# Kernel tuning notes

Hardware: AMD Instinct MI355X
Metric: run time of the kernel (lower is better)

Reference implementation:

```python
import jax, jax.numpy as jnp
import numpy as np

D_MODEL = 1024
NUM_HEADS = 16
D_K = D_MODEL // NUM_HEADS
S, B = 2048, 2


def setup_inputs() -> dict:
    key = jax.random.key(0)
    ks = jax.random.split(key, 11)
    lim = 1.0 / np.sqrt(D_MODEL)
    def lin(kw, kb):
        W = jax.random.uniform(kw, (D_MODEL, D_MODEL), jnp.float32, -lim, lim)
        b = jax.random.uniform(kb, (D_MODEL,), jnp.float32, -lim, lim)
        return W, b
    Wq, bq = lin(ks[0], ks[1])
    Wk, bk = lin(ks[2], ks[3])
    Wv, bv = lin(ks[4], ks[5])
    Wo, bo = lin(ks[6], ks[7])
    q = jax.random.normal(ks[8], (S, B, D_MODEL), jnp.float32)
    k = jax.random.normal(ks[9], (S, B, D_MODEL), jnp.float32)
    v = jax.random.normal(ks[10], (S, B, D_MODEL), jnp.float32)
    return {"q": q, "k": k, "v": v,
            "Wq": Wq, "bq": bq, "Wk": Wk, "bk": bk,
            "Wv": Wv, "bv": bv, "Wo": Wo, "bo": bo}


def reference(q, k, v, Wq, bq, Wk, bk, Wv, bv, Wo, bo):
    s, b, _ = q.shape
    scale = np.sqrt(D_K).astype(np.float32)
    # torch Linear: x @ W.T + b
    def proj(x, W, bias):
        y = jnp.einsum('sbd,ed->sbe', x, W) + bias
        # [S,B,D] -> [B,H,S,d_k]
        return y.reshape(s, b, NUM_HEADS, D_K).transpose(1, 2, 0, 3)
    Q = proj(q, Wq, bq)
    K = proj(k, Wk, bk)
    V = proj(v, Wv, bv)
    scores = jnp.einsum('bhsd,bhtd->bhst', Q, K) / scale  # [B,H,S,S]
    attn = jax.nn.softmax(scores, axis=-1)
    ctx = jnp.einsum('bhst,bhtd->bhsd', attn, V)  # [B,H,S,d_k]
    ctx = ctx.transpose(2, 0, 1, 3).reshape(s, b, NUM_HEADS * D_K)
    return jnp.einsum('sbd,ed->sbe', ctx, Wo) + bo
```

## Files before the change

### kernel.cpp

```cpp
#include <hip/hip_runtime.h>
#include <stdint.h>

typedef __attribute__((ext_vector_type(8))) short short8;
typedef __attribute__((ext_vector_type(4))) float f32x4;
typedef __attribute__((ext_vector_type(16))) float f32x16;

#define MFMA16(a, b, c) __builtin_amdgcn_mfma_f32_16x16x32_bf16((a), (b), (c), 0, 0, 0)
#define MFMA32(a, b, c) __builtin_amdgcn_mfma_f32_32x32x16_bf16((a), (b), (c), 0, 0, 0)

__device__ inline unsigned short f2bf(float x) {
  unsigned u = __float_as_uint(x);
  u = (u + 0x7FFFu + ((u >> 16) & 1u)) >> 16;
  return (unsigned short)u;
}

__device__ inline void gload16(const unsigned short* g, unsigned short* l) {
  __builtin_amdgcn_global_load_lds(
      (const __attribute__((address_space(1))) unsigned int*)g,
      (__attribute__((address_space(3))) unsigned int*)l, 16, 0, 0);
}

__device__ inline short8 lds8(const unsigned short* base, int byteoff) {
  return *reinterpret_cast<const short8*>(reinterpret_cast<const char*>(base) + byteoff);
}

__device__ inline unsigned cvtpk(float lo, float hi) {
  unsigned r;
  asm("v_cvt_pk_bf16_f32 %0, %1, %2" : "=v"(r) : "v"(lo), "v"(hi));
  return r;
}
__device__ inline void plswap(unsigned& a, unsigned& b) {
  asm volatile("v_permlane32_swap_b32 %0, %1" : "+v"(a), "+v"(b));
}

__device__ inline short8 mk8(unsigned a, unsigned b, unsigned c, unsigned d) {
  union { unsigned u[4]; short8 v; } x;
  x.u[0] = a; x.u[1] = b; x.u[2] = c; x.u[3] = d;
  return x.v;
}

__device__ inline int swz(int row, int chunk) {
  return row * 128 + (((chunk) ^ (row & 7)) << 4);
}

__global__ __launch_bounds__(256) void cvt_bf16x(const float* __restrict__ a0,
                                                 const float* __restrict__ a1,
                                                 const float* __restrict__ a2,
                                                 const float* __restrict__ a3,
                                                 unsigned short* __restrict__ d, int per) {
  int y = blockIdx.y;
  const float* s = (y == 0) ? a0 : (y == 1) ? a1 : (y == 2) ? a2 : a3;
  int i = (blockIdx.x * 256 + threadIdx.x) * 8;
  if (i >= per) return;
  float4 v0 = *reinterpret_cast<const float4*>(s + i);
  float4 v1 = *reinterpret_cast<const float4*>(s + i + 4);
  short8 o;
  o[0] = (short)f2bf(v0.x); o[1] = (short)f2bf(v0.y);
  o[2] = (short)f2bf(v0.z); o[3] = (short)f2bf(v0.w);
  o[4] = (short)f2bf(v1.x); o[5] = (short)f2bf(v1.y);
  o[6] = (short)f2bf(v1.z); o[7] = (short)f2bf(v1.w);
  *reinterpret_cast<short8*>(d + (size_t)y * per + i) = o;
}

template <int MODE>
__global__ __launch_bounds__(256) void gemm_bt(
    const unsigned short* __restrict__ Abase, const unsigned short* __restrict__ Wbase,
    const float* __restrict__ bias0, const float* __restrict__ bias1,
    const float* __restrict__ bias2, unsigned short* __restrict__ ObaseBf,
    float* __restrict__ ObaseF, int M, int N, int K) {
  constexpr int CHUNK = (MODE == 0) ? 96 : 32;
  const int orig = blockIdx.x;
  const int wg = (orig & 7) * CHUNK + (orig >> 3);
  int z, bx, by;
  if (MODE == 0) {
    z = wg >> 8; by = (wg >> 5) & 7; bx = wg & 31;
  } else {
    z = 0; by = wg >> 5; bx = wg & 31;
  }

  const unsigned short* A = Abase + (size_t)z * M * K;
  const unsigned short* W = Wbase + (size_t)z * N * K;
  const float* bias = (z == 0) ? bias0 : (z == 1 ? bias1 : bias2);

  __shared__ unsigned short As[128 * 64];
  __shared__ unsigned short Bs[128 * 64];

  const int t = threadIdx.x;
  const int lane = t & 63, w = t >> 6;
  const int wm = w >> 1, wn = w & 1;
  const int m0 = bx * 128, n0 = by * 128;
  const int lrow = lane & 15, lg = lane >> 4;

  f32x4 acc[4][4] = {};

  for (int kt = 0; kt < K; kt += 64) {
    __syncthreads();
#pragma unroll
    for (int p = 0; p < 4; ++p) {
      int ci = (p * 4 + w) * 64;
      int c = ci + lane;
      int row = c >> 3, cc = (c & 7) ^ (row & 7);
      gload16(&A[(size_t)(m0 + row) * K + kt + cc * 8], &As[ci * 8]);
      gload16(&W[(size_t)(n0 + row) * K + kt + cc * 8], &Bs[ci * 8]);
    }
    __syncthreads();
#pragma unroll
    for (int kc = 0; kc < 2; ++kc) {
      short8 af[4], bfr[4];
#pragma unroll
      for (int i = 0; i < 4; ++i) {
        af[i] = *reinterpret_cast<const short8*>((const char*)As + swz(wm * 64 + i * 16 + lrow, kc * 4 + lg));
        bfr[i] = *reinterpret_cast<const short8*>((const char*)Bs + swz(wn * 64 + i * 16 + lrow, kc * 4 + lg));
      }
#pragma unroll
      for (int mi = 0; mi < 4; ++mi)
#pragma unroll
        for (int ni = 0; ni < 4; ++ni) acc[mi][ni] = MFMA16(af[mi], bfr[ni], acc[mi][ni]);
    }
  }

  const int r0 = lg * 4;
  if (MODE == 0) {
    const float scale = (z == 0) ? 0.18033688011112042f : 1.0f;
    if (z < 2) {
      unsigned short* O = ObaseBf + (size_t)z * (size_t)M * N;
#pragma unroll
      for (int mi = 0; mi < 4; ++mi)
#pragma unroll
        for (int ni = 0; ni < 4; ++ni) {
          int e = n0 + wn * 64 + ni * 16 + lrow;
          float be = bias[e];
          int h = e >> 6, d = e & 63;
#pragma unroll
          for (int r = 0; r < 4; ++r) {
            int m = m0 + wm * 64 + mi * 16 + r0 + r;
            int s = m >> 1, bb = m & 1;
            O[(((size_t)(bb * 16 + h) * 2048 + s) << 6) + d] = f2bf((acc[mi][ni][r] + be) * scale);
          }
        }
    } else {
      unsigned short* O = ObaseBf + (size_t)2 * (size_t)M * N;
#pragma unroll
      for (int mi = 0; mi < 4; ++mi)
#pragma unroll
        for (int ni = 0; ni < 4; ++ni) {
          int e = n0 + wn * 64 + ni * 16 + lrow;
          float be = bias[e];
          int h = e >> 6, d = e & 63;
#pragma unroll
          for (int r = 0; r < 4; ++r) {
            int m = m0 + wm * 64 + mi * 16 + r0 + r;
            int s = m >> 1, bb = m & 1;
            O[(((size_t)(bb * 16 + h) * 64 + d) << 11) + s] = f2bf(acc[mi][ni][r] + be);
          }
        }
    }
  } else {
    float* O = ObaseF;
#pragma unroll
    for (int mi = 0; mi < 4; ++mi)
#pragma unroll
      for (int ni = 0; ni < 4; ++ni) {
        int e = n0 + wn * 64 + ni * 16 + lrow;
        float be = bias[e];
#pragma unroll
        for (int r = 0; r < 4; ++r) {
          int m = m0 + wm * 64 + mi * 16 + r0 + r;
          O[(size_t)m * N + e] = acc[mi][ni][r] + be;
        }
      }
  }
}

__global__ __launch_bounds__(256) void attn(const unsigned short* __restrict__ Q,
                                            const unsigned short* __restrict__ K,
                                            const unsigned short* __restrict__ Vt,
                                            unsigned short* __restrict__ ctx) {
  __shared__ unsigned short Ks[4 * 4096];
  __shared__ unsigned short Vs[4 * 4096];

  const int orig = blockIdx.x;
  const int wg = ((orig & 7) << 6) + (orig >> 3);
  const int bh = wg >> 4;
  const int qb = wg & 15;

  const int t = threadIdx.x, lane = t & 63, wv = t >> 6;
  const int q0 = qb * 128 + wv * 32;
  const int q = lane & 31, hi = lane >> 5;
  const int fq = (q ^ (q >> 3)) & 7;

  const unsigned short* Qb = Q + ((size_t)bh * 2048 + q0) * 64;
  const unsigned short* Kb = K + (size_t)bh * 2048 * 64;
  const unsigned short* Vb = Vt + (size_t)bh * 64 * 2048;

  short8 qf[4];
#pragma unroll
  for (int m = 0; m < 4; ++m)
    qf[m] = *reinterpret_cast<const short8*>(&Qb[q * 64 + m * 16 + hi * 8]);

  const short8 ones = {0x3F80, 0x3F80, 0x3F80, 0x3F80, 0x3F80, 0x3F80, 0x3F80, 0x3F80};

  int koff[2][4], voff[2][2][2];
#pragma unroll
  for (int st = 0; st < 2; ++st) {
    int f = fq ^ (st ? 4 : 0);
#pragma unroll
    for (int m = 0; m < 4; ++m)
      koff[st][m] = (st * 32 + q) * 128 + (((m * 2 + hi) ^ f) << 4);
  }
#pragma unroll
  for (int dh = 0; dh < 2; ++dh) {
    int f = fq ^ (dh ? 4 : 0);
#pragma unroll
    for (int st = 0; st < 2; ++st)
#pragma unroll
      for (int kc = 0; kc < 2; ++kc)
        voff[dh][st][kc] = (dh * 32 + q) * 128 + (((st * 4 + kc * 2 + hi) ^ f) << 4);
  }

  int c0 = wv * 64 + lane, c1 = (4 + wv) * 64 + lane;
  int sr0 = c0 >> 3, sr1 = c1 >> 3;
  int sc0c = ((c0 & 7) ^ ((sr0 ^ (sr0 >> 3)) & 7)) * 8;
  int sc1c = ((c1 & 7) ^ ((sr1 ^ (sr1 >> 3)) & 7)) * 8;
  const unsigned short* ks0 = Kb + (size_t)sr0 * 64 + sc0c;
  const unsigned short* ks1 = Kb + (size_t)sr1 * 64 + sc1c;
  const unsigned short* vp0 = Vb + (size_t)sr0 * 2048 + sc0c;
  const unsigned short* vp1 = Vb + (size_t)sr1 * 2048 + sc1c;

  f32x16 oa0 = {}, oa1 = {}, osum = {};

#pragma unroll
  for (int pt = 0; pt < 3; ++pt) {
    char* kb = (char*)Ks + pt * 8192;
    char* vb2 = (char*)Vs + pt * 8192;
    gload16(ks0, (unsigned short*)(kb + wv * 1024));
    gload16(ks1, (unsigned short*)(kb + (4 + wv) * 1024));
    gload16(vp0, (unsigned short*)(vb2 + wv * 1024));
    gload16(vp1, (unsigned short*)(vb2 + (4 + wv) * 1024));
    ks0 += 4096; ks1 += 4096; vp0 += 64; vp1 += 64;
  }

  for (int tile = 0; tile < 32; ++tile) {
    asm volatile("s_waitcnt vmcnt(8)" ::: "memory");
    __builtin_amdgcn_s_barrier();
    __builtin_amdgcn_sched_barrier(0);

    {
      char* kb = (char*)Ks + ((tile + 3) & 3) * 8192;
      char* vb2 = (char*)Vs + ((tile + 3) & 3) * 8192;
      gload16(ks0, (unsigned short*)(kb + wv * 1024));
      gload16(ks1, (unsigned short*)(kb + (4 + wv) * 1024));
      gload16(vp0, (unsigned short*)(vb2 + wv * 1024));
      gload16(vp1, (unsigned short*)(vb2 + (4 + wv) * 1024));
      ks0 += 4096; ks1 += 4096; vp0 += 64; vp1 += 64;
    }

    const int cur = (tile & 3) * 8192;
    __builtin_amdgcn_s_setprio(1);

    f32x16 s0 = {}, s1 = {};
#pragma unroll
    for (int m = 0; m < 4; ++m) {
      short8 k0 = lds8(Ks, cur + koff[0][m]);
      short8 k1 = lds8(Ks, cur + koff[1][m]);
      s0 = MFMA32(k0, qf[m], s0);
      s1 = MFMA32(k1, qf[m], s1);
    }

#pragma unroll
    for (int st = 0; st < 2; ++st) {
      const f32x16& sv = st ? s1 : s0;
      float p[16];
#pragma unroll
      for (int i = 0; i < 16; ++i) p[i] = __builtin_amdgcn_exp2f(sv[i]);

      unsigned w0 = cvtpk(p[0], p[1]), w1 = cvtpk(p[2], p[3]);
      unsigned w2 = cvtpk(p[4], p[5]), w3 = cvtpk(p[6], p[7]);
      plswap(w0, w2); plswap(w1, w3);
      unsigned w4 = cvtpk(p[8], p[9]), w5 = cvtpk(p[10], p[11]);
      unsigned w6 = cvtpk(p[12], p[13]), w7 = cvtpk(p[14], p[15]);
      plswap(w4, w6); plswap(w5, w7);
      short8 pa0 = mk8(w0, w1, w2, w3);
      short8 pa1 = mk8(w4, w5, w6, w7);

      osum = MFMA32(pa0, ones, osum);
      oa0 = MFMA32(pa0, lds8(Vs, cur + voff[0][st][0]), oa0);
      oa1 = MFMA32(pa0, lds8(Vs, cur + voff[1][st][0]), oa1);
      osum = MFMA32(pa1, ones, osum);
      oa0 = MFMA32(pa1, lds8(Vs, cur + voff[0][st][1]), oa0);
      oa1 = MFMA32(pa1, lds8(Vs, cur + voff[1][st][1]), oa1);
    }
    __builtin_amdgcn_s_setprio(0);
  }

  const int b = bh >> 4, h = bh & 15;
#pragma unroll
  for (int r = 0; r < 16; ++r) {
    int qr = (r & 3) + 8 * (r >> 2) + 4 * hi;
    float li = 1.0f / osum[r];
    size_t base = ((size_t)(q0 + qr) * 2 + b) * 1024 + h * 64 + q;
    ctx[base] = f2bf(oa0[r] * li);
    ctx[base + 32] = f2bf(oa1[r] * li);
  }
}

extern "C" void kernel_launch(void* const* d_in, const int* in_sizes, int n_in, void* d_out,
                              int out_size, void* d_ws, size_t ws_size, hipStream_t stream) {
  const float* q  = (const float*)d_in[0];
  const float* k  = (const float*)d_in[1];
  const float* v  = (const float*)d_in[2];
  const float* Wq = (const float*)d_in[3];
  const float* bq = (const float*)d_in[4];
  const float* Wk = (const float*)d_in[5];
  const float* bk = (const float*)d_in[6];
  const float* Wv = (const float*)d_in[7];
  const float* bv = (const float*)d_in[8];
  const float* Wo = (const float*)d_in[9];
  const float* bo = (const float*)d_in[10];

  const size_t SZ_IN = 4194304;
  const size_t SZ_W  = 1048576;
  unsigned short* ws  = (unsigned short*)d_ws;
  unsigned short* xb  = ws;
  unsigned short* Wb  = xb + 3 * SZ_IN;
  unsigned short* QKV = Wb + 4 * SZ_W;
  unsigned short* ctx = QKV + 3 * SZ_IN;

  cvt_bf16x<<<dim3(SZ_IN / 2048, 3), 256, 0, stream>>>(q, k, v, v, xb, (int)SZ_IN);
  cvt_bf16x<<<dim3(SZ_W / 2048, 4), 256, 0, stream>>>(Wq, Wk, Wv, Wo, Wb, (int)SZ_W);

  gemm_bt<0><<<768, 256, 0, stream>>>(xb, Wb, bq, bk, bv, QKV, nullptr, 4096, 1024, 1024);
  attn<<<512, 256, 0, stream>>>(QKV, QKV + SZ_IN, QKV + 2 * SZ_IN, ctx);
  gemm_bt<1><<<256, 256, 0, stream>>>(ctx, Wb + 3 * SZ_W, bo, bo, bo, nullptr,
                                      (float*)d_out, 4096, 1024, 1024);
}
```

Measured before the change: 141.7 us.

## Double-buffer GEMM LDS tiles and halve output GEMM tile width

The GEMM kernel now double-buffers its LDS tiles, issuing the next K-slice's global-to-LDS loads before the MFMA work on the current slice, with one barrier per iteration instead of two. The output projection uses 128x64 tiles and a grid of 512 blocks instead of 256, which puts more workgroups across the CUs. The cost is twice the LDS per block, which may lower occupancy, plus one wasted prefetch of slice 0 on the final iteration. The MODE 1 block mapping is also changed (by = wg>>5 now covers 16 column tiles), and it stays consistent with the new CHUNK of 64.

```diff
diff --git a/kernel.cpp b/kernel.cpp
--- a/kernel.cpp
+++ b/kernel.cpp
@@ -68,7 +68,11 @@
     const float* __restrict__ bias0, const float* __restrict__ bias1,
     const float* __restrict__ bias2, unsigned short* __restrict__ ObaseBf,
     float* __restrict__ ObaseF, int M, int N, int K) {
-  constexpr int CHUNK = (MODE == 0) ? 96 : 32;
+  constexpr int BN = (MODE == 0) ? 128 : 64;
+  constexpr int WN = BN / 32;
+  constexpr int CB = BN / 32;
+  constexpr int CHUNK = (MODE == 0) ? 96 : 64;
+
   const int orig = blockIdx.x;
   const int wg = (orig & 7) * CHUNK + (orig >> 3);
   int z, bx, by;
@@ -82,42 +86,70 @@
   const unsigned short* W = Wbase + (size_t)z * N * K;
   const float* bias = (z == 0) ? bias0 : (z == 1 ? bias1 : bias2);
 
-  __shared__ unsigned short As[128 * 64];
-  __shared__ unsigned short Bs[128 * 64];
+  __shared__ unsigned short As[2 * 128 * 64];
+  __shared__ unsigned short Bs[2 * BN * 64];
 
   const int t = threadIdx.x;
   const int lane = t & 63, w = t >> 6;
   const int wm = w >> 1, wn = w & 1;
-  const int m0 = bx * 128, n0 = by * 128;
+  const int m0 = bx * 128, n0 = by * BN;
   const int lrow = lane & 15, lg = lane >> 4;
 
-  f32x4 acc[4][4] = {};
-
+  f32x4 acc[4][WN] = {};
+
+  int arow[4], acol[4], brow[CB], bcol[CB];
+#pragma unroll
+  for (int p = 0; p < 4; ++p) {
+    int c = (p * 4 + w) * 64 + lane;
+    arow[p] = c >> 3; acol[p] = ((c & 7) ^ (arow[p] & 7)) * 8;
+  }
+#pragma unroll
+  for (int p = 0; p < CB; ++p) {
+    int c = (p * 4 + w) * 64 + lane;
+    brow[p] = c >> 3; bcol[p] = ((c & 7) ^ (brow[p] & 7)) * 8;
+  }
+
+#define STAGE_G(kt, buf)                                                              \
+  {                                                                                   \
+    _Pragma("unroll") for (int p = 0; p < 4; ++p)                                     \
+        gload16(&A[(size_t)(m0 + arow[p]) * K + (kt) + acol[p]],                      \
+                &As[(buf)*8192 + ((p * 4 + w) * 64) * 8]);                            \
+    _Pragma("unroll") for (int p = 0; p < CB; ++p)                                    \
+        gload16(&W[(size_t)(n0 + brow[p]) * K + (kt) + bcol[p]],                      \
+                &Bs[(buf)*BN * 64 + ((p * 4 + w) * 64) * 8]);                         \
+  }
+
+  STAGE_G(0, 0);
+  asm volatile("s_waitcnt vmcnt(0)" ::: "memory");
+  __builtin_amdgcn_s_barrier();
+  __builtin_amdgcn_sched_barrier(0);
+
+  int cur = 0;
   for (int kt = 0; kt < K; kt += 64) {
-    __syncthreads();
-#pragma unroll
-    for (int p = 0; p < 4; ++p) {
-      int ci = (p * 4 + w) * 64;
-      int c = ci + lane;
-      int row = c >> 3, cc = (c & 7) ^ (row & 7);
-      gload16(&A[(size_t)(m0 + row) * K + kt + cc * 8], &As[ci * 8]);
-      gload16(&W[(size_t)(n0 + row) * K + kt + cc * 8], &Bs[ci * 8]);
-    }
-    __syncthreads();
+    int ktn = (kt + 64 < K) ? kt + 64 : 0;
+    STAGE_G(ktn, cur ^ 1);
+
 #pragma unroll
     for (int kc = 0; kc < 2; ++kc) {
-      short8 af[4], bfr[4];
-#pragma unroll
-      for (int i = 0; i < 4; ++i) {
-        af[i] = *reinterpret_cast<const short8*>((const char*)As + swz(wm * 64 + i * 16 + lrow, kc * 4 + lg));
-        bfr[i] = *reinterpret_cast<const short8*>((const char*)Bs + swz(wn * 64 + i * 16 + lrow, kc * 4 + lg));
-      }
+      short8 af[4], bfr[WN];
+#pragma unroll
+      for (int i = 0; i < 4; ++i)
+        af[i] = lds8(As, cur * 16384 + swz(wm * 64 + i * 16 + lrow, kc * 4 + lg));
+#pragma unroll
+      for (int i = 0; i < WN; ++i)
+        bfr[i] = lds8(Bs, cur * BN * 128 + swz(wn * (BN / 2) + i * 16 + lrow, kc * 4 + lg));
 #pragma unroll
       for (int mi = 0; mi < 4; ++mi)
 #pragma unroll
-        for (int ni = 0; ni < 4; ++ni) acc[mi][ni] = MFMA16(af[mi], bfr[ni], acc[mi][ni]);
-    }
-  }
+        for (int ni = 0; ni < WN; ++ni) acc[mi][ni] = MFMA16(af[mi], bfr[ni], acc[mi][ni]);
+    }
+
+    asm volatile("s_waitcnt vmcnt(0)" ::: "memory");
+    __builtin_amdgcn_s_barrier();
+    __builtin_amdgcn_sched_barrier(0);
+    cur ^= 1;
+  }
+#undef STAGE_G
 
   const int r0 = lg * 4;
   if (MODE == 0) {
@@ -160,8 +192,8 @@
 #pragma unroll
     for (int mi = 0; mi < 4; ++mi)
 #pragma unroll
-      for (int ni = 0; ni < 4; ++ni) {
-        int e = n0 + wn * 64 + ni * 16 + lrow;
+      for (int ni = 0; ni < WN; ++ni) {
+        int e = n0 + wn * 32 + ni * 16 + lrow;
         float be = bias[e];
 #pragma unroll
         for (int r = 0; r < 4; ++r) {
@@ -331,6 +363,6 @@
 
   gemm_bt<0><<<768, 256, 0, stream>>>(xb, Wb, bq, bk, bv, QKV, nullptr, 4096, 1024, 1024);
   attn<<<512, 256, 0, stream>>>(QKV, QKV + SZ_IN, QKV + 2 * SZ_IN, ctx);
-  gemm_bt<1><<<256, 256, 0, stream>>>(ctx, Wb + 3 * SZ_W, bo, bo, bo, nullptr,
+  gemm_bt<1><<<512, 256, 0, stream>>>(ctx, Wb + 3 * SZ_W, bo, bo, bo, nullptr,
                                       (float*)d_out, 4096, 1024, 1024);
 }
```

Result: slower. 153.6 us (+8.4%).
